# Performance work log

Hardware: AMD Instinct MI355X
Metric: run time of the kernel (lower is better)

The kernel has to match this reference:

```python
import jax, jax.numpy as jnp
import numpy as np
from jax import lax

H = 64          # num_heads
P = 64          # head_dim
N = 128         # ssm_state_size
G = 8           # n_groups
K = 4           # conv_kernel
D_MODEL = 4096  # hidden_size
I = H * P                      # intermediate_size = 4096
GN = G * N                     # groups_time_state_size = 1024
CONV_DIM = I + 2 * GN          # 6144
PROJ = I + CONV_DIM + H        # 10304
EPS = 1e-5
GROUP_SIZE = I // G            # 512


def setup_inputs() -> dict:
    key = jax.random.key(0)
    ks = jax.random.split(key, 6)
    B, L = 2, 2048
    s = 0.02
    return {
        "hidden_states": jax.random.normal(ks[0], (B, L, D_MODEL), jnp.float32),
        "in_proj_w": jax.random.normal(ks[1], (PROJ, D_MODEL), jnp.float32) * s,
        "conv_weight": jax.random.normal(ks[2], (CONV_DIM, K), jnp.float32) * s,
        "conv_bias": jnp.zeros((CONV_DIM,), jnp.float32),
        "dt_bias": jnp.ones((H,), jnp.float32),
        "A_log": jnp.log(jnp.arange(1, H + 1, dtype=jnp.float32)),
        "D": jnp.ones((H,), jnp.float32),
        "norm_weight": jnp.ones((I,), jnp.float32),
        "out_proj_w": jax.random.normal(ks[3], (D_MODEL, I), jnp.float32) * s,
    }


def reference(hidden_states, in_proj_w, conv_weight, conv_bias, dt_bias, A_log, D, norm_weight, out_proj_w):
    B, L, _ = hidden_states.shape

    # in_proj, then split into gate / conv-stream / dt
    proj = jnp.einsum("bld,pd->blp", hidden_states, in_proj_w)
    gate = proj[..., :I]
    hbc = proj[..., I:I + CONV_DIM]          # (B, L, conv_dim), pre-conv
    dt = proj[..., -H:]                       # (B, L, H)

    # depthwise causal conv1d + SiLU
    pad = jnp.pad(hbc, ((0, 0), (K - 1, 0), (0, 0)))
    conv = conv_bias
    for k in range(K):  # K=4, tiny fixed loop
        conv = conv + pad[:, k:k + L, :] * conv_weight[:, k]
    xBC = jax.nn.silu(conv)

    x = xBC[..., :I].reshape(B, L, H, P)                        # (B,L,H,P)
    Bm = xBC[..., I:I + GN].reshape(B, L, G, N)
    Cm = xBC[..., I + GN:].reshape(B, L, G, N)
    hpg = H // G
    B_h = jnp.repeat(Bm, hpg, axis=2)                            # (B,L,H,N)
    C_h = jnp.repeat(Cm, hpg, axis=2)                            # (B,L,H,N)

    # dt processing: softplus(dt + dt_bias), limits (0, inf)
    dt_p = jax.nn.softplus(dt + dt_bias)                         # (B,L,H)
    A = -jnp.exp(A_log)                                          # (H,)
    dA = jnp.exp(dt_p * A)                                       # (B,L,H)
    dtx = dt_p[..., None] * x                                    # (B,L,H,P)

    # selective scan over sequence (O(L)), state: (B,H,P,N)
    def step(state, inp):
        dA_t, dtx_t, B_t, C_t = inp
        state = state * dA_t[..., None, None] + dtx_t[..., None] * B_t[:, :, None, :]
        y_t = jnp.einsum("bhpn,bhn->bhp", state, C_t)
        return state, y_t

    xs = (jnp.moveaxis(dA, 1, 0), jnp.moveaxis(dtx, 1, 0),
          jnp.moveaxis(B_h, 1, 0), jnp.moveaxis(C_h, 1, 0))
    state0 = jnp.zeros((B, H, P, N), jnp.float32)
    final_state, ys = lax.scan(step, state0, xs)
    y = jnp.moveaxis(ys, 0, 1) + x * D[None, None, :, None]      # (B,L,H,P)
    y = y.reshape(B, L, I)

    # gated grouped RMSNorm: 8 independent RMSNorms over 512 elems each
    yg = y.reshape(B, L, G, GROUP_SIZE)
    var = jnp.mean(yg * yg, axis=-1, keepdims=True)
    yn = (yg * lax.rsqrt(var + EPS)).reshape(B, L, I) * norm_weight
    yn = yn * jax.nn.silu(gate)

    out = jnp.einsum("bli,di->bld", yn, out_proj_w)

    conv_state_new = jnp.moveaxis(hbc[:, L - (K - 1):, :], 1, 2)  # (B, conv_dim, K-1)
    return out, conv_state_new, final_state
```

## Files before the change

### kernel.cpp

```cpp
#include <hip/hip_runtime.h>
#include <cstdint>
#include <cstddef>

typedef __bf16 bf16;
typedef float f32x4 __attribute__((ext_vector_type(4)));
typedef bf16 bf16x8 __attribute__((ext_vector_type(8)));
typedef bf16 bf16x4 __attribute__((ext_vector_type(4)));

#define DM    4096
#define LL    2048
#define BB    2
#define BT    4096
#define II    4096
#define GN_   1024
#define CONVD 6144
#define PROJD 10304
#define NPAD  10496
#define HH    64
#define PP    64
#define NN    128
#define CT    64
#define NC    32

#define OUT_OFS_CONV  16777216
#define OUT_OFS_STATE 16814080

#define WS_HSB    0UL
#define WS_WINB   33554432UL
#define WS_DSB    0UL
#define WS_PROJ   119537664UL
#define WS_XBC    291504128UL
#define WS_DTDA   392167424UL
#define WS_Y      394264576UL
#define WS_WOUTB  0UL
#define WS_YNB    33554432UL

__device__ __forceinline__ void gl2lds16(const void* g, void* l) {
  __builtin_amdgcn_global_load_lds(
      (__attribute__((address_space(1))) unsigned int*)(uintptr_t)g,
      (__attribute__((address_space(3))) unsigned int*)(uintptr_t)l, 16, 0, 0);
}

__global__ __launch_bounds__(256) void cast2_kernel(const float* __restrict__ s1,
                                                    bf16* __restrict__ d1,
                                                    const float* __restrict__ s2,
                                                    bf16* __restrict__ d2,
                                                    long nsrc2, long ndst2) {
  if (blockIdx.x < 16384) {
    long i = ((long)blockIdx.x * 256 + threadIdx.x) * 4;
    float4 v = *(const float4*)(s1 + i);
    bf16x4 o;
    o[0] = (bf16)v.x; o[1] = (bf16)v.y; o[2] = (bf16)v.z; o[3] = (bf16)v.w;
    *(bf16x4*)(d1 + i) = o;
  } else {
    long i = ((long)(blockIdx.x - 16384) * 256 + threadIdx.x) * 4;
    if (i >= ndst2) return;
    bf16x4 o;
    if (i < nsrc2) {
      float4 v = *(const float4*)(s2 + i);
      o[0] = (bf16)v.x; o[1] = (bf16)v.y; o[2] = (bf16)v.z; o[3] = (bf16)v.w;
    } else {
      o[0] = (bf16)0.f; o[1] = (bf16)0.f; o[2] = (bf16)0.f; o[3] = (bf16)0.f;
    }
    *(bf16x4*)(d2 + i) = o;
  }
}

__global__ __launch_bounds__(256) void cast_kernel(const float* __restrict__ src,
                                                   bf16* __restrict__ dst,
                                                   long nsrc, long ndst) {
  long i = ((long)blockIdx.x * 256 + threadIdx.x) * 4;
  if (i >= ndst) return;
  bf16x4 o;
  if (i < nsrc) {
    float4 v = *(const float4*)(src + i);
    o[0] = (bf16)v.x; o[1] = (bf16)v.y; o[2] = (bf16)v.z; o[3] = (bf16)v.w;
  } else {
    o[0] = (bf16)0.f; o[1] = (bf16)0.f; o[2] = (bf16)0.f; o[3] = (bf16)0.f;
  }
  *(bf16x4*)(dst + i) = o;
}

#define BARF() do { asm volatile("" ::: "memory");                    \
                    __builtin_amdgcn_s_barrier();                     \
                    asm volatile("" ::: "memory"); } while (0)
#define WAITLGKM0() do { asm volatile("s_waitcnt lgkmcnt(0)" ::: "memory"); \
                         __builtin_amdgcn_sched_barrier(0); } while (0)
#define HINTLGKM8() asm volatile("s_waitcnt lgkmcnt(8)" ::: "memory")
#define WAITVM(n) asm volatile("s_waitcnt vmcnt(" #n ")" ::: "memory")
#define PRIO1 __builtin_amdgcn_s_setprio(1)
#define PRIO0 __builtin_amdgcn_s_setprio(0)

__device__ __forceinline__ void stage_A_half(const bf16* __restrict__ A, int K,
                                             int arow, int kt, bf16* lds,
                                             int h, int tid) {
#pragma unroll
  for (int j = 0; j < 2; ++j) {
    const int r  = h * 64 + j * 128 + (tid >> 3);
    const int cb = (tid & 7) * 16;
    const int cs = cb ^ ((r & 7) << 4);
    gl2lds16(A + (size_t)(arow + r) * K + kt * 64 + (cs >> 1),
             lds + r * 64 + (cb >> 1));
  }
}
__device__ __forceinline__ void stage_B_half(const bf16* __restrict__ B, int K,
                                             int brow, int kt, bf16* lds,
                                             int h, int tid) {
#pragma unroll
  for (int j = 0; j < 2; ++j) {
    const int quarter = j * 2 + (tid >> 8);
    const int kq = tid & 255;
    const int r  = quarter * 64 + h * 32 + (kq >> 3);
    const int cb = (kq & 7) * 16;
    const int cs = cb ^ ((r & 7) << 4);
    gl2lds16(B + (size_t)(brow + r) * K + kt * 64 + (cs >> 1),
             lds + r * 64 + (cb >> 1));
  }
}

#define LDA4(p, mh) do {                                                     \
  _Pragma("unroll") for (int mt = 0; mt < 4; ++mt)                           \
  _Pragma("unroll") for (int kk = 0; kk < 2; ++kk) {                         \
    const int rr = wm * 128 + (mh) * 64 + mt * 16 + l16;                     \
    const int cc = (kk * 64 + quad * 16) ^ ((rr & 7) << 4);                  \
    a_[mt][kk] = *(const bf16x8*)((const char*)(&sA[p][rr][0]) + cc);        \
  } } while (0)

#define LDB2(p, np, barr) do {                                               \
  _Pragma("unroll") for (int nt = 0; nt < 2; ++nt)                           \
  _Pragma("unroll") for (int kk = 0; kk < 2; ++kk) {                         \
    const int rr = wn * 64 + (np) * 32 + nt * 16 + l16;                      \
    const int cc = (kk * 64 + quad * 16) ^ ((rr & 7) << 4);                  \
    barr[nt][kk] = *(const bf16x8*)((const char*)(&sB[p][rr][0]) + cc);      \
  } } while (0)

#define MFMAQ(mh, barr, nb0) do {                                            \
  _Pragma("unroll") for (int kk = 0; kk < 2; ++kk)                           \
  _Pragma("unroll") for (int mt = 0; mt < 4; ++mt)                           \
  _Pragma("unroll") for (int nt = 0; nt < 2; ++nt)                           \
    acc[(mh) * 4 + mt][(nb0) + nt] = __builtin_amdgcn_mfma_f32_16x16x32_bf16(\
        a_[mt][kk], barr[nt][kk], acc[(mh) * 4 + mt][(nb0) + nt], 0, 0, 0);  \
  } while (0)

__global__ __launch_bounds__(512, 2) void gemm256(const bf16* __restrict__ A,
                                                  const bf16* __restrict__ B,
                                                  float* __restrict__ C,
                                                  int M, int N, int K, int NB) {
  __shared__ __align__(16) bf16 sA[2][256][64];
  __shared__ __align__(16) bf16 sB[2][256][64];

  const int tid  = threadIdx.x;
  const int wave = tid >> 6, lane = tid & 63;
  const int l16  = lane & 15, quad = lane >> 4;
  const int wm   = wave >> 2, wn = wave & 3;

  const int nwg = gridDim.x;
  const int q = nwg >> 3, r8 = nwg & 7;
  const int xcd = blockIdx.x & 7, idx = blockIdx.x >> 3;
  const int wgid = (xcd < r8 ? xcd * (q + 1) : r8 * (q + 1) + (xcd - r8) * q) + idx;
  const int mb = wgid / NB, nb = wgid - mb * NB;
  const int arow = mb * 256, brow = nb * 256;

  f32x4 acc[8][4];
#pragma unroll
  for (int i = 0; i < 8; ++i)
#pragma unroll
    for (int j = 0; j < 4; ++j) acc[i][j] = (f32x4)0.f;

  const int NT = K >> 6;

  stage_A_half(A, K, arow, 0, &sA[0][0][0], 0, tid);
  stage_B_half(B, K, brow, 0, &sB[0][0][0], 0, tid);
  stage_A_half(A, K, arow, 0, &sA[0][0][0], 1, tid);
  stage_B_half(B, K, brow, 0, &sB[0][0][0], 1, tid);
  stage_A_half(A, K, arow, 1, &sA[1][0][0], 0, tid);
  stage_B_half(B, K, brow, 1, &sB[1][0][0], 0, tid);
  stage_A_half(A, K, arow, 1, &sA[1][0][0], 1, tid);
  WAITVM(6);
  BARF();

  bf16x8 a_[4][2], b0_[2][2], b1_[2][2];

  for (int i = 0; i < NT / 2; ++i) {
    const int t1o = 2 * i + 1;
    const int t2  = (2 * i + 2 < NT) ? 2 * i + 2 : NT - 1;
    const int t3  = (2 * i + 3 < NT) ? 2 * i + 3 : NT - 1;

    LDA4(0, 0); LDB2(0, 0, b0_);
    stage_B_half(B, K, brow, t1o, &sB[1][0][0], 1, tid);
    HINTLGKM8();
    BARF(); WAITLGKM0();
    PRIO1; MFMAQ(0, b0_, 0); PRIO0;
    BARF();
    LDB2(0, 1, b1_);
    stage_A_half(A, K, arow, t2, &sA[0][0][0], 0, tid);
    BARF(); WAITLGKM0();
    PRIO1; MFMAQ(0, b1_, 2); PRIO0;
    BARF();
    LDA4(0, 1);
    stage_B_half(B, K, brow, t2, &sB[0][0][0], 0, tid);
    BARF(); WAITLGKM0();
    PRIO1; MFMAQ(1, b1_, 2); PRIO0;
    BARF();
    stage_A_half(A, K, arow, t2, &sA[0][0][0], 1, tid);
    WAITVM(6);
    BARF();
    PRIO1; MFMAQ(1, b0_, 0); PRIO0;
    BARF();
    LDA4(1, 0); LDB2(1, 0, b0_);
    stage_B_half(B, K, brow, t2, &sB[0][0][0], 1, tid);
    HINTLGKM8();
    BARF(); WAITLGKM0();
    PRIO1; MFMAQ(0, b0_, 0); PRIO0;
    BARF();
    LDB2(1, 1, b1_);
    stage_A_half(A, K, arow, t3, &sA[1][0][0], 0, tid);
    BARF(); WAITLGKM0();
    PRIO1; MFMAQ(0, b1_, 2); PRIO0;
    BARF();
    LDA4(1, 1);
    stage_B_half(B, K, brow, t3, &sB[1][0][0], 0, tid);
    BARF(); WAITLGKM0();
    PRIO1; MFMAQ(1, b1_, 2); PRIO0;
    BARF();
    stage_A_half(A, K, arow, t3, &sA[1][0][0], 1, tid);
    WAITVM(6);
    BARF();
    PRIO1; MFMAQ(1, b0_, 0); PRIO0;
    BARF();
  }
  asm volatile("s_waitcnt vmcnt(0)" ::: "memory");
  __builtin_amdgcn_s_barrier();

#pragma unroll
  for (int mt = 0; mt < 8; ++mt) {
    const int row0 = arow + wm * 128 + mt * 16 + quad * 4;
#pragma unroll
    for (int nt = 0; nt < 4; ++nt) {
      const int col = brow + wn * 64 + nt * 16 + l16;
#pragma unroll
      for (int r = 0; r < 4; ++r)
        C[(size_t)(row0 + r) * N + col] = acc[mt][nt][r];
    }
  }
}

#define CTILE 64
__global__ __launch_bounds__(256) void conv_kernel(const float* __restrict__ proj,
                                                   const float* __restrict__ cw,
                                                   const float* __restrict__ cb,
                                                   bf16* __restrict__ xbc) {
  const int c   = blockIdx.x * 256 + threadIdx.x;
  const int bt0 = blockIdx.y * CTILE;
  const int t0  = bt0 & (LL - 1);
  const float4 w = *(const float4*)(cw + c * 4);
  const float bias = cb[c];
  const float* p = proj + (size_t)bt0 * NPAD + II + c;
  float h0, h1, h2;
  if (t0 == 0) {
    h0 = 0.f; h1 = 0.f; h2 = 0.f;
  } else {
    h0 = p[-3 * (ptrdiff_t)NPAD];
    h1 = p[-2 * (ptrdiff_t)NPAD];
    h2 = p[-(ptrdiff_t)NPAD];
  }
  bf16* q = xbc + (size_t)bt0 * CONVD + c;
#pragma unroll 8
  for (int t = 0; t < CTILE; ++t) {
    const float cur = p[(ptrdiff_t)t * NPAD];
    const float acc = bias + h0 * w.x + h1 * w.y + h2 * w.z + cur * w.w;
    q[(size_t)t * CONVD] = (bf16)(acc / (1.f + __expf(-acc)));
    h0 = h1; h1 = h2; h2 = cur;
  }
}

__global__ __launch_bounds__(256) void dtcs_kernel(const float* __restrict__ proj,
                                                   const float* __restrict__ dt_bias,
                                                   const float* __restrict__ A_log,
                                                   float* __restrict__ dtda,
                                                   float* __restrict__ outp) {
  const int bid = blockIdx.x;
  if (bid < 1024) {
    const int idx = bid * 256 + threadIdx.x;
    const int bt = idx >> 6, h = idx & 63;
    const float z = proj[(size_t)bt * NPAD + (II + CONVD) + h] + dt_bias[h];
    const float sp = (z > 20.f) ? z : log1pf(__expf(z));
    const float a = -__expf(A_log[h]);
    float2 o; o.x = sp; o.y = __expf(sp * a);
    *(float2*)(dtda + (size_t)idx * 2) = o;
  } else {
    const int idx = (bid - 1024) * 256 + threadIdx.x;
    if (idx >= BB * CONVD * 3) return;
    const int b = idx / (CONVD * 3);
    const int r = idx - b * CONVD * 3;
    const int c = r / 3, j = r - c * 3;
    outp[idx] = proj[((size_t)b * LL + (LL - 3 + j)) * NPAD + II + c];
  }
}

#define SCAN_DECODE()                                                  \
  const int lin = blockIdx.x;                                          \
  const int hh  = (lin >> 3) & 7;                                      \
  const int id  = (lin & 7) | ((lin >> 6) << 3);                       \
  const int g   = id >> 6, c = (id >> 1) & 31, b = id & 1;             \
  const int h   = g * 8 + hh;

__global__ __launch_bounds__(256) void chunkA_kernel(const bf16* __restrict__ xbc,
                                                     const float* __restrict__ dtda,
                                                     const float* __restrict__ A_log,
                                                     float* __restrict__ ybuf,
                                                     bf16* __restrict__ dsb) {
  SCAN_DECODE();
  const int tid = threadIdx.x;
  const int wave = tid >> 6, lane = tid & 63;
  const int l16 = lane & 15, quad = lane >> 4;

  __shared__ __align__(16) bf16 CsBt[8192];
  __shared__ __align__(16) bf16 Bs[64][128];
  __shared__ __align__(16) bf16 Xt[64][64];
  __shared__ __align__(16) bf16 Ws[64][64];
  __shared__ float cums[64], dtps[64], wls[64];

  bf16 (*Cs)[128] = (bf16(*)[128])CsBt;
  bf16 (*Bt)[64]  = (bf16(*)[64])CsBt;

  const size_t rowbase = ((size_t)b * LL + (size_t)c * CT) * CONVD;

  {
    const int r0 = wave * 16;
    const bf16* gC = xbc + rowbase + (II + GN_) + g * 128;
    const bf16* gB = xbc + rowbase + II + g * 128;
#pragma unroll
    for (int j = 0; j < 4; ++j) {
      const int r  = r0 + j * 4 + (lane >> 4);
      const int ch = (lane & 15) ^ (r & 15);
      gl2lds16(gC + (size_t)r * CONVD + ch * 8, &Cs[r0 + j * 4][0]);
      gl2lds16(gB + (size_t)r * CONVD + ch * 8, &Bs[r0 + j * 4][0]);
    }
  }
  {
    const int j = tid >> 2, p0 = (tid & 3) * 16;
    const bf16* gpX = xbc + rowbase + (size_t)j * CONVD + h * 64 + p0;
#pragma unroll
    for (int k = 0; k < 2; ++k) {
      bf16x8 v = *(const bf16x8*)(gpX + k * 8);
#pragma unroll
      for (int e = 0; e < 8; ++e) {
        const int pp = p0 + k * 8 + e;
        Xt[pp][(((j >> 3) ^ (pp & 7)) * 8) + (j & 7)] = v[e];
      }
    }
  }
  if (wave == 0) {
    const float Ah = -__expf(A_log[h]);
    float2 dd = *(const float2*)(dtda + ((size_t)((b * LL + c * CT + lane)) * 64 + h) * 2);
    float s = dd.x * Ah;
#pragma unroll
    for (int d = 1; d < 64; d <<= 1) {
      float v = __shfl_up(s, d);
      if (lane >= d) s += v;
    }
    const float tot = __shfl(s, 63);
    cums[lane] = s;
    dtps[lane] = dd.x;
    wls[lane]  = __expf(tot - s) * dd.x;
  }
  __syncthreads();

  const int mrow = wave * 16 + l16;
  {
    f32x4 accg[4];
#pragma unroll
    for (int nt = 0; nt < 4; ++nt) accg[nt] = (f32x4)0.f;
#pragma unroll
    for (int k0 = 0; k0 < 128; k0 += 32) {
      bf16x8 af = *(const bf16x8*)&Cs[mrow][(((k0 >> 3) + quad) ^ (mrow & 15)) * 8];
#pragma unroll
      for (int nt = 0; nt < 4; ++nt) {
        const int nrow = nt * 16 + l16;
        bf16x8 bfr = *(const bf16x8*)&Bs[nrow][(((k0 >> 3) + quad) ^ (nrow & 15)) * 8];
        accg[nt] = __builtin_amdgcn_mfma_f32_16x16x32_bf16(af, bfr, accg[nt], 0, 0, 0);
      }
    }
#pragma unroll
    for (int nt = 0; nt < 4; ++nt) {
      const int j = nt * 16 + l16;
#pragma unroll
      for (int r = 0; r < 4; ++r) {
        const int i = wave * 16 + quad * 4 + r;
        float v = 0.f;
        if (j <= i) v = accg[nt][r] * __expf(cums[i] - cums[j]) * dtps[j];
        Ws[i][(((j >> 3) ^ (i & 7)) * 8) + (j & 7)] = (bf16)v;
      }
    }
  }
  __syncthreads();

  {
    const int n = tid >> 1, j0 = (tid & 1) * 32;
#pragma unroll
    for (int k = 0; k < 4; ++k) {
      bf16x8 v;
#pragma unroll
      for (int e = 0; e < 8; ++e) {
        const int j = j0 + k * 8 + e;
        v[e] = Bs[j][(((n >> 3) ^ (j & 15)) * 8) + (n & 7)];
      }
      *(bf16x8*)(&Bt[n][((((j0 + k * 8) >> 3) ^ (n & 7)) * 8)]) = v;
    }
  }
  __syncthreads();

  f32x4 accy[4];
#pragma unroll
  for (int pt = 0; pt < 4; ++pt) accy[pt] = (f32x4)0.f;
#pragma unroll
  for (int k0 = 0; k0 < 64; k0 += 32) {
    bf16x8 af = *(const bf16x8*)&Ws[mrow][(((k0 >> 3) + quad) ^ (mrow & 7)) * 8];
#pragma unroll
    for (int pt = 0; pt < 4; ++pt) {
      const int prow = pt * 16 + l16;
      bf16x8 bfr = *(const bf16x8*)&Xt[prow][(((k0 >> 3) + quad) ^ (prow & 7)) * 8];
      accy[pt] = __builtin_amdgcn_mfma_f32_16x16x32_bf16(af, bfr, accy[pt], 0, 0, 0);
    }
  }

  f32x4 accs[8];
#pragma unroll
  for (int nt = 0; nt < 8; ++nt) accs[nt] = (f32x4)0.f;
#pragma unroll
  for (int k0 = 0; k0 < 64; k0 += 32) {
    bf16x8 axr = *(const bf16x8*)&Xt[mrow][(((k0 >> 3) + quad) ^ (mrow & 7)) * 8];
    bf16x8 ax;
#pragma unroll
    for (int e = 0; e < 8; ++e)
      ax[e] = (bf16)((float)axr[e] * wls[k0 + quad * 8 + e]);
#pragma unroll
    for (int nt = 0; nt < 8; ++nt) {
      const int nrow = nt * 16 + l16;
      bf16x8 bfr = *(const bf16x8*)&Bt[nrow][(((k0 >> 3) + quad) ^ (nrow & 7)) * 8];
      accs[nt] = __builtin_amdgcn_mfma_f32_16x16x32_bf16(ax, bfr, accs[nt], 0, 0, 0);
    }
  }

#pragma unroll
  for (int pt = 0; pt < 4; ++pt) {
#pragma unroll
    for (int r = 0; r < 4; ++r) {
      const int i = wave * 16 + quad * 4 + r;
      ybuf[((size_t)(b * LL + c * CT + i)) * II + h * 64 + pt * 16 + l16] = accy[pt][r];
    }
  }
  const size_t dbase = (((size_t)(b * HH + h)) * NC + c) * (CT * NN);
#pragma unroll
  for (int nt = 0; nt < 8; ++nt) {
#pragma unroll
    for (int r = 0; r < 4; ++r) {
      const int p = wave * 16 + quad * 4 + r;
      dsb[dbase + (size_t)p * NN + nt * 16 + l16] = (bf16)accs[nt][r];
    }
  }
}

__global__ __launch_bounds__(256) void chain_kernel(const float* __restrict__ dtda,
                                                    const float* __restrict__ A_log,
                                                    bf16* __restrict__ dsb,
                                                    float* __restrict__ fst) {
  const int blk = blockIdx.x;
  const int b = blk >> 8, h = (blk >> 2) & 63, qtr = blk & 3;
  const int tid = threadIdx.x, wave = tid >> 6, lane = tid & 63;
  __shared__ float DcL[NC];

  const float Ah = -__expf(A_log[h]);
#pragma unroll
  for (int cc = 0; cc < 8; ++cc) {
    const int c = wave * 8 + cc;
    float2 dd = *(const float2*)(dtda + ((size_t)(b * LL + c * CT + lane) * 64 + h) * 2);
    float a = dd.x * Ah;
#pragma unroll
    for (int m = 1; m <= 32; m <<= 1) a += __shfl_xor(a, m);
    if (lane == 0) DcL[c] = __expf(a);
  }

  const int local = qtr * 2048 + tid * 8;
  const size_t base = ((size_t)(b * HH + h)) * NC * (CT * NN) + local;
  float s[8];
#pragma unroll
  for (int e = 0; e < 8; ++e) s[e] = 0.f;

  bf16x8 d0 = *(const bf16x8*)(dsb + base);
  __syncthreads();

  for (int c = 0; c < NC; ++c) {
    bf16* p = dsb + base + (size_t)c * (CT * NN);
    bf16x8 dn;
    if (c + 1 < NC) dn = *(const bf16x8*)(p + (CT * NN));
    const float dc = DcL[c];
    bf16x8 o0;
#pragma unroll
    for (int e = 0; e < 8; ++e) o0[e] = (bf16)s[e];
    *(bf16x8*)(p) = o0;
#pragma unroll
    for (int e = 0; e < 8; ++e) s[e] = s[e] * dc + (float)d0[e];
    d0 = dn;
  }
  float* fp = fst + ((size_t)(b * HH + h)) * (PP * NN) + local;
#pragma unroll
  for (int k = 0; k < 2; ++k) {
    float4 v = { s[k * 4], s[k * 4 + 1], s[k * 4 + 2], s[k * 4 + 3] };
    *(float4*)(fp + k * 4) = v;
  }
}

__global__ __launch_bounds__(256) void chunkB_kernel(const bf16* __restrict__ xbc,
                                                     const float* __restrict__ dtda,
                                                     const float* __restrict__ A_log,
                                                     const float* __restrict__ Dv,
                                                     const bf16* __restrict__ spb,
                                                     float* __restrict__ ybuf) {
  SCAN_DECODE();
  const int tid = threadIdx.x;
  const int wave = tid >> 6, lane = tid & 63;
  const int l16 = lane & 15, quad = lane >> 4;

  __shared__ __align__(16) bf16 Cs[64][128];
  __shared__ __align__(16) bf16 Sp[64][128];
  __shared__ float es[64];

  const size_t rowbase = ((size_t)b * LL + (size_t)c * CT) * CONVD;
  {
    const int r0 = wave * 16;
    const bf16* gC = xbc + rowbase + (II + GN_) + g * 128;
    const bf16* gS = spb + (((size_t)(b * HH + h)) * NC + c) * (CT * NN);
#pragma unroll
    for (int j = 0; j < 4; ++j) {
      const int r  = r0 + j * 4 + (lane >> 4);
      const int ch = (lane & 15) ^ (r & 15);
      gl2lds16(gC + (size_t)r * CONVD + ch * 8, &Cs[r0 + j * 4][0]);
      gl2lds16(gS + (size_t)r * NN   + ch * 8, &Sp[r0 + j * 4][0]);
    }
  }
  if (wave == 0) {
    const float Ah = -__expf(A_log[h]);
    float2 dd = *(const float2*)(dtda + ((size_t)(b * LL + c * CT + lane) * 64 + h) * 2);
    float s = dd.x * Ah;
#pragma unroll
    for (int d = 1; d < 64; d <<= 1) {
      float v = __shfl_up(s, d);
      if (lane >= d) s += v;
    }
    es[lane] = __expf(s);
  }
  __syncthreads();

  const int mrow = wave * 16 + l16;
  f32x4 acc[4];
#pragma unroll
  for (int pt = 0; pt < 4; ++pt) acc[pt] = (f32x4)0.f;
#pragma unroll
  for (int k0 = 0; k0 < 128; k0 += 32) {
    bf16x8 af = *(const bf16x8*)&Cs[mrow][(((k0 >> 3) + quad) ^ (mrow & 15)) * 8];
#pragma unroll
    for (int pt = 0; pt < 4; ++pt) {
      const int prow = pt * 16 + l16;
      bf16x8 bfr = *(const bf16x8*)&Sp[prow][(((k0 >> 3) + quad) ^ (prow & 15)) * 8];
      acc[pt] = __builtin_amdgcn_mfma_f32_16x16x32_bf16(af, bfr, acc[pt], 0, 0, 0);
    }
  }

  const float Dh = Dv[h];
#pragma unroll
  for (int pt = 0; pt < 4; ++pt) {
#pragma unroll
    for (int r = 0; r < 4; ++r) {
      const int i = wave * 16 + quad * 4 + r;
      const int p = pt * 16 + l16;
      const size_t row = (size_t)(b * LL + c * CT + i);
      const size_t ya = row * II + h * 64 + p;
      const float xv = (float)xbc[row * CONVD + h * 64 + p];
      ybuf[ya] = acc[pt][r] * es[i] + ybuf[ya] + Dh * xv;
    }
  }
}

__global__ __launch_bounds__(256) void norm_kernel(const float* __restrict__ y,
                                                   const float* __restrict__ proj,
                                                   const float* __restrict__ nw,
                                                   bf16* __restrict__ yn) {
  const int bt = blockIdx.x, tid = threadIdx.x;
  const float* yr = y + (size_t)bt * II + tid * 16;
  float4 v[4];
  float ss = 0.f;
#pragma unroll
  for (int i = 0; i < 4; ++i) {
    v[i] = *(const float4*)(yr + i * 4);
    ss += v[i].x * v[i].x + v[i].y * v[i].y + v[i].z * v[i].z + v[i].w * v[i].w;
  }
#pragma unroll
  for (int m = 1; m <= 16; m <<= 1) ss += __shfl_xor(ss, m);
  const float rstd = rsqrtf(ss * (1.f / 512.f) + 1e-5f);

  const float* gr  = proj + (size_t)bt * NPAD + tid * 16;
  const float* nwr = nw + tid * 16;
  bf16x8 o0, o1;
#pragma unroll
  for (int i = 0; i < 4; ++i) {
    float4 gv = *(const float4*)(gr + i * 4);
    float4 nv = *(const float4*)(nwr + i * 4);
    const float* vv = (const float*)&v[i];
    const float* gg = (const float*)&gv;
    const float* nn = (const float*)&nv;
#pragma unroll
    for (int j = 0; j < 4; ++j) {
      const float gate = gg[j];
      const float val = vv[j] * rstd * nn[j] * (gate / (1.f + __expf(-gate)));
      if (i < 2) o0[i * 4 + j] = (bf16)val;
      else       o1[(i - 2) * 4 + j] = (bf16)val;
    }
  }
  bf16* dst = yn + (size_t)bt * II + tid * 16;
  *(bf16x8*)(dst)     = o0;
  *(bf16x8*)(dst + 8) = o1;
}

extern "C" void kernel_launch(void* const* d_in, const int* in_sizes, int n_in,
                              void* d_out, int out_size, void* d_ws, size_t ws_size,
                              hipStream_t stream) {
  const float* hs      = (const float*)d_in[0];
  const float* w_in    = (const float*)d_in[1];
  const float* cw      = (const float*)d_in[2];
  const float* cb      = (const float*)d_in[3];
  const float* dt_bias = (const float*)d_in[4];
  const float* A_log   = (const float*)d_in[5];
  const float* Dv      = (const float*)d_in[6];
  const float* nw      = (const float*)d_in[7];
  const float* w_out   = (const float*)d_in[8];

  char* ws = (char*)d_ws;
  bf16*  hsb   = (bf16*)(ws + WS_HSB);
  bf16*  winb  = (bf16*)(ws + WS_WINB);
  bf16*  dsb   = (bf16*)(ws + WS_DSB);
  float* proj  = (float*)(ws + WS_PROJ);
  bf16*  xbc   = (bf16*)(ws + WS_XBC);
  float* dtda  = (float*)(ws + WS_DTDA);
  float* ybuf  = (float*)(ws + WS_Y);
  bf16*  ynb   = (bf16*)(ws + WS_YNB);
  bf16*  woutb = (bf16*)(ws + WS_WOUTB);

  float* outp = (float*)d_out;

  cast2_kernel<<<58368, 256, 0, stream>>>(hs, hsb, w_in, winb,
                                          (long)PROJD * DM, (long)NPAD * DM);

  gemm256<<<(BT / 256) * (NPAD / 256), 512, 0, stream>>>(hsb, winb, proj, BT, NPAD, DM, NPAD / 256);

  conv_kernel<<<dim3(CONVD / 256, BT / CTILE), 256, 0, stream>>>(proj, cw, cb, xbc);
  dtcs_kernel<<<1168, 256, 0, stream>>>(proj, dt_bias, A_log, dtda, outp + OUT_OFS_CONV);

  chunkA_kernel<<<4096, 256, 0, stream>>>(xbc, dtda, A_log, ybuf, dsb);
  chain_kernel<<<BB * HH * 4, 256, 0, stream>>>(dtda, A_log, dsb, outp + OUT_OFS_STATE);
  chunkB_kernel<<<4096, 256, 0, stream>>>(xbc, dtda, A_log, Dv, dsb, ybuf);

  cast_kernel<<<16384, 256, 0, stream>>>(w_out, woutb, 16777216L, 16777216L);
  norm_kernel<<<BT, 256, 0, stream>>>(ybuf, proj, nw, ynb);

  gemm256<<<(BT / 256) * (DM / 256), 512, 0, stream>>>(ynb, woutb, outp, BT, DM, II, DM / 256);
}
```

Measured before the change: 962.2 us.

## Store projection in bf16 and fuse chunk output with grouped RMSNorm gating

```diff
diff --git a/kernel.cpp b/kernel.cpp
--- a/kernel.cpp
+++ b/kernel.cpp
@@ -28,12 +28,14 @@
 #define WS_HSB    0UL
 #define WS_WINB   33554432UL
 #define WS_DSB    0UL
+#define WS_YNB    67108864UL
 #define WS_PROJ   119537664UL
-#define WS_XBC    291504128UL
-#define WS_DTDA   392167424UL
-#define WS_Y      394264576UL
-#define WS_WOUTB  0UL
-#define WS_YNB    33554432UL
+#define WS_XBC    205520896UL
+#define WS_DTDA   255852544UL
+#define WS_Y      257949696UL
+#define WS_DTF    291504128UL
+#define WS_HBC3   292552704UL
+#define WS_WOUTB  292700160UL
 
 __device__ __forceinline__ void gl2lds16(const void* g, void* l) {
   __builtin_amdgcn_global_load_lds(
@@ -41,19 +43,22 @@
       (__attribute__((address_space(3))) unsigned int*)(uintptr_t)l, 16, 0, 0);
 }
 
-__global__ __launch_bounds__(256) void cast2_kernel(const float* __restrict__ s1,
+__global__ __launch_bounds__(256) void cast3_kernel(const float* __restrict__ s1,
                                                     bf16* __restrict__ d1,
                                                     const float* __restrict__ s2,
                                                     bf16* __restrict__ d2,
+                                                    const float* __restrict__ s3,
+                                                    bf16* __restrict__ d3,
                                                     long nsrc2, long ndst2) {
-  if (blockIdx.x < 16384) {
-    long i = ((long)blockIdx.x * 256 + threadIdx.x) * 4;
+  const int bid = blockIdx.x;
+  if (bid < 16384) {
+    long i = ((long)bid * 256 + threadIdx.x) * 4;
     float4 v = *(const float4*)(s1 + i);
     bf16x4 o;
     o[0] = (bf16)v.x; o[1] = (bf16)v.y; o[2] = (bf16)v.z; o[3] = (bf16)v.w;
     *(bf16x4*)(d1 + i) = o;
-  } else {
-    long i = ((long)(blockIdx.x - 16384) * 256 + threadIdx.x) * 4;
+  } else if (bid < 58368) {
+    long i = ((long)(bid - 16384) * 256 + threadIdx.x) * 4;
     if (i >= ndst2) return;
     bf16x4 o;
     if (i < nsrc2) {
@@ -63,22 +68,13 @@
       o[0] = (bf16)0.f; o[1] = (bf16)0.f; o[2] = (bf16)0.f; o[3] = (bf16)0.f;
     }
     *(bf16x4*)(d2 + i) = o;
-  }
-}
-
-__global__ __launch_bounds__(256) void cast_kernel(const float* __restrict__ src,
-                                                   bf16* __restrict__ dst,
-                                                   long nsrc, long ndst) {
-  long i = ((long)blockIdx.x * 256 + threadIdx.x) * 4;
-  if (i >= ndst) return;
-  bf16x4 o;
-  if (i < nsrc) {
-    float4 v = *(const float4*)(src + i);
+  } else {
+    long i = ((long)(bid - 58368) * 256 + threadIdx.x) * 4;
+    float4 v = *(const float4*)(s3 + i);
+    bf16x4 o;
     o[0] = (bf16)v.x; o[1] = (bf16)v.y; o[2] = (bf16)v.z; o[3] = (bf16)v.w;
-  } else {
-    o[0] = (bf16)0.f; o[1] = (bf16)0.f; o[2] = (bf16)0.f; o[3] = (bf16)0.f;
-  }
-  *(bf16x4*)(dst + i) = o;
+    *(bf16x4*)(d3 + i) = o;
+  }
 }
 
 #define BARF() do { asm volatile("" ::: "memory");                    \
@@ -142,10 +138,13 @@
         a_[mt][kk], barr[nt][kk], acc[(mh) * 4 + mt][(nb0) + nt], 0, 0, 0);  \
   } while (0)
 
+template <int MODE>
 __global__ __launch_bounds__(512, 2) void gemm256(const bf16* __restrict__ A,
                                                   const bf16* __restrict__ B,
-                                                  float* __restrict__ C,
-                                                  int M, int N, int K, int NB) {
+                                                  void* __restrict__ Cv,
+                                                  int M, int N, int K, int NB,
+                                                  float* __restrict__ dtf,
+                                                  float* __restrict__ hbc3) {
   __shared__ __align__(16) bf16 sA[2][256][64];
   __shared__ __align__(16) bf16 sB[2][256][64];
 
@@ -239,14 +238,26 @@
     for (int nt = 0; nt < 4; ++nt) {
       const int col = brow + wn * 64 + nt * 16 + l16;
 #pragma unroll
-      for (int r = 0; r < 4; ++r)
-        C[(size_t)(row0 + r) * N + col] = acc[mt][nt][r];
+      for (int r = 0; r < 4; ++r) {
+        const float v = acc[mt][nt][r];
+        const int row = row0 + r;
+        if constexpr (MODE == 0) {
+          ((float*)Cv)[(size_t)row * N + col] = v;
+        } else {
+          ((bf16*)Cv)[(size_t)row * N + col] = (bf16)v;
+          const int dc = col - (II + CONVD);
+          if (dc >= 0 && dc < 64) dtf[(size_t)row * 64 + dc] = v;
+          const int rr = row & (LL - 1);
+          if (rr >= LL - 3 && col >= II && col < II + CONVD)
+            hbc3[((size_t)(row >> 11) * 3 + (rr - (LL - 3))) * CONVD + (col - II)] = v;
+        }
+      }
     }
   }
 }
 
 #define CTILE 64
-__global__ __launch_bounds__(256) void conv_kernel(const float* __restrict__ proj,
+__global__ __launch_bounds__(256) void conv_kernel(const bf16* __restrict__ proj,
                                                    const float* __restrict__ cw,
                                                    const float* __restrict__ cb,
                                                    bf16* __restrict__ xbc) {
@@ -255,26 +266,27 @@
   const int t0  = bt0 & (LL - 1);
   const float4 w = *(const float4*)(cw + c * 4);
   const float bias = cb[c];
-  const float* p = proj + (size_t)bt0 * NPAD + II + c;
+  const bf16* p = proj + (size_t)bt0 * NPAD + II + c;
   float h0, h1, h2;
   if (t0 == 0) {
     h0 = 0.f; h1 = 0.f; h2 = 0.f;
   } else {
-    h0 = p[-3 * (ptrdiff_t)NPAD];
-    h1 = p[-2 * (ptrdiff_t)NPAD];
-    h2 = p[-(ptrdiff_t)NPAD];
+    h0 = (float)p[-3 * (ptrdiff_t)NPAD];
+    h1 = (float)p[-2 * (ptrdiff_t)NPAD];
+    h2 = (float)p[-(ptrdiff_t)NPAD];
   }
   bf16* q = xbc + (size_t)bt0 * CONVD + c;
 #pragma unroll 8
   for (int t = 0; t < CTILE; ++t) {
-    const float cur = p[(ptrdiff_t)t * NPAD];
+    const float cur = (float)p[(ptrdiff_t)t * NPAD];
     const float acc = bias + h0 * w.x + h1 * w.y + h2 * w.z + cur * w.w;
     q[(size_t)t * CONVD] = (bf16)(acc / (1.f + __expf(-acc)));
     h0 = h1; h1 = h2; h2 = cur;
   }
 }
 
-__global__ __launch_bounds__(256) void dtcs_kernel(const float* __restrict__ proj,
+__global__ __launch_bounds__(256) void dtcs_kernel(const float* __restrict__ dtf,
+                                                   const float* __restrict__ hbc3,
                                                    const float* __restrict__ dt_bias,
                                                    const float* __restrict__ A_log,
                                                    float* __restrict__ dtda,
@@ -282,8 +294,8 @@
   const int bid = blockIdx.x;
   if (bid < 1024) {
     const int idx = bid * 256 + threadIdx.x;
-    const int bt = idx >> 6, h = idx & 63;
-    const float z = proj[(size_t)bt * NPAD + (II + CONVD) + h] + dt_bias[h];
+    const int h = idx & 63;
+    const float z = dtf[idx] + dt_bias[h];
     const float sp = (z > 20.f) ? z : log1pf(__expf(z));
     const float a = -__expf(A_log[h]);
     float2 o; o.x = sp; o.y = __expf(sp * a);
@@ -294,7 +306,7 @@
     const int b = idx / (CONVD * 3);
     const int r = idx - b * CONVD * 3;
     const int c = r / 3, j = r - c * 3;
-    outp[idx] = proj[((size_t)b * LL + (LL - 3 + j)) * NPAD + II + c];
+    outp[idx] = hbc3[((size_t)b * 3 + j) * CONVD + c];
   }
 }
 
@@ -308,7 +320,7 @@
 __global__ __launch_bounds__(256) void chunkA_kernel(const bf16* __restrict__ xbc,
                                                      const float* __restrict__ dtda,
                                                      const float* __restrict__ A_log,
-                                                     float* __restrict__ ybuf,
+                                                     bf16* __restrict__ ybuf,
                                                      bf16* __restrict__ dsb) {
   SCAN_DECODE();
   const int tid = threadIdx.x;
@@ -448,7 +460,7 @@
 #pragma unroll
     for (int r = 0; r < 4; ++r) {
       const int i = wave * 16 + quad * 4 + r;
-      ybuf[((size_t)(b * LL + c * CT + i)) * II + h * 64 + pt * 16 + l16] = accy[pt][r];
+      ybuf[((size_t)(b * LL + c * CT + i)) * II + h * 64 + pt * 16 + l16] = (bf16)accy[pt][r];
     }
   }
   const size_t dbase = (((size_t)(b * HH + h)) * NC + c) * (CT * NN);
@@ -512,35 +524,52 @@
   }
 }
 
-__global__ __launch_bounds__(256) void chunkB_kernel(const bf16* __restrict__ xbc,
-                                                     const float* __restrict__ dtda,
-                                                     const float* __restrict__ A_log,
-                                                     const float* __restrict__ Dv,
-                                                     const bf16* __restrict__ spb,
-                                                     float* __restrict__ ybuf) {
-  SCAN_DECODE();
+__global__ __launch_bounds__(512) void chunkBN_kernel(const bf16* __restrict__ xbc,
+                                                      const float* __restrict__ dtda,
+                                                      const float* __restrict__ A_log,
+                                                      const float* __restrict__ Dv,
+                                                      const bf16* __restrict__ spb,
+                                                      const bf16* __restrict__ ybi,
+                                                      const bf16* __restrict__ proj,
+                                                      const float* __restrict__ nw,
+                                                      bf16* __restrict__ ynb) {
+  const int lin = blockIdx.x;
+  const int g = lin >> 6, c = (lin >> 1) & 31, b = lin & 1;
   const int tid = threadIdx.x;
-  const int wave = tid >> 6, lane = tid & 63;
+  const int w = tid >> 6, lane = tid & 63;
   const int l16 = lane & 15, quad = lane >> 4;
-
-  __shared__ __align__(16) bf16 Cs[64][128];
-  __shared__ __align__(16) bf16 Sp[64][128];
+  const int h = g * 8 + w;
+
+  __shared__ __align__(16) char LB[147456];
+  __shared__ float sums[8][64];
   __shared__ float es[64];
+  __shared__ float rstd[64];
+
+  bf16 (*Cs)[128] = (bf16(*)[128])LB;
+  bf16 (*Sp)[128] = (bf16(*)[128])(LB + 16384 + (size_t)w * 16384);
 
   const size_t rowbase = ((size_t)b * LL + (size_t)c * CT) * CONVD;
   {
-    const int r0 = wave * 16;
     const bf16* gC = xbc + rowbase + (II + GN_) + g * 128;
+#pragma unroll
+    for (int j = 0; j < 2; ++j) {
+      const int r  = w * 8 + j * 4 + (lane >> 4);
+      const int ch = (lane & 15) ^ (r & 15);
+      gl2lds16(gC + (size_t)r * CONVD + ch * 8, LB + (w * 8 + j * 4) * 256);
+    }
     const bf16* gS = spb + (((size_t)(b * HH + h)) * NC + c) * (CT * NN);
 #pragma unroll
-    for (int j = 0; j < 4; ++j) {
-      const int r  = r0 + j * 4 + (lane >> 4);
+    for (int j = 0; j < 16; ++j) {
+      const int r  = j * 4 + (lane >> 4);
       const int ch = (lane & 15) ^ (r & 15);
-      gl2lds16(gC + (size_t)r * CONVD + ch * 8, &Cs[r0 + j * 4][0]);
-      gl2lds16(gS + (size_t)r * NN   + ch * 8, &Sp[r0 + j * 4][0]);
-    }
-  }
-  if (wave == 0) {
+      gl2lds16(gS + (size_t)r * NN + ch * 8, LB + 16384 + w * 16384 + j * 1024);
+    }
+  }
+  if (w == 0) {
+    const float Ah = -__expf(A_log[h]);
+  }
+  __shared__ float esw[8][64];
+  {
     const float Ah = -__expf(A_log[h]);
     float2 dd = *(const float2*)(dtda + ((size_t)(b * LL + c * CT + lane) * 64 + h) * 2);
     float s = dd.x * Ah;
@@ -549,78 +578,108 @@
       float v = __shfl_up(s, d);
       if (lane >= d) s += v;
     }
-    es[lane] = __expf(s);
+    esw[w][lane] = __expf(s);
   }
   __syncthreads();
 
-  const int mrow = wave * 16 + l16;
-  f32x4 acc[4];
-#pragma unroll
-  for (int pt = 0; pt < 4; ++pt) acc[pt] = (f32x4)0.f;
+  f32x4 acc[4][4];
+#pragma unroll
+  for (int it = 0; it < 4; ++it)
+#pragma unroll
+    for (int pt = 0; pt < 4; ++pt) acc[it][pt] = (f32x4)0.f;
+
 #pragma unroll
   for (int k0 = 0; k0 < 128; k0 += 32) {
-    bf16x8 af = *(const bf16x8*)&Cs[mrow][(((k0 >> 3) + quad) ^ (mrow & 15)) * 8];
-#pragma unroll
-    for (int pt = 0; pt < 4; ++pt) {
-      const int prow = pt * 16 + l16;
-      bf16x8 bfr = *(const bf16x8*)&Sp[prow][(((k0 >> 3) + quad) ^ (prow & 15)) * 8];
-      acc[pt] = __builtin_amdgcn_mfma_f32_16x16x32_bf16(af, bfr, acc[pt], 0, 0, 0);
-    }
+    bf16x8 af[4], bfr[4];
+#pragma unroll
+    for (int it = 0; it < 4; ++it) {
+      const int rr = it * 16 + l16;
+      af[it]  = *(const bf16x8*)&Cs[rr][(((k0 >> 3) + quad) ^ (rr & 15)) * 8];
+      bfr[it] = *(const bf16x8*)&Sp[rr][(((k0 >> 3) + quad) ^ (rr & 15)) * 8];
+    }
+#pragma unroll
+    for (int it = 0; it < 4; ++it)
+#pragma unroll
+      for (int pt = 0; pt < 4; ++pt)
+        acc[it][pt] = __builtin_amdgcn_mfma_f32_16x16x32_bf16(af[it], bfr[pt], acc[it][pt], 0, 0, 0);
   }
 
   const float Dh = Dv[h];
-#pragma unroll
-  for (int pt = 0; pt < 4; ++pt) {
+  const size_t grow0 = (size_t)b * LL + (size_t)c * CT;
+#pragma unroll
+  for (int it = 0; it < 4; ++it)
+#pragma unroll
+    for (int pt = 0; pt < 4; ++pt)
+#pragma unroll
+      for (int r = 0; r < 4; ++r) {
+        const int row = it * 16 + quad * 4 + r;
+        const int colh = pt * 16 + l16;
+        const size_t gr = grow0 + row;
+        acc[it][pt][r] = acc[it][pt][r] * esw[w][row]
+                       + (float)ybi[gr * II + h * 64 + colh]
+                       + Dh * (float)xbc[gr * CONVD + h * 64 + colh];
+      }
+
+  float ssv[4][4];
+#pragma unroll
+  for (int it = 0; it < 4; ++it)
 #pragma unroll
     for (int r = 0; r < 4; ++r) {
-      const int i = wave * 16 + quad * 4 + r;
-      const int p = pt * 16 + l16;
-      const size_t row = (size_t)(b * LL + c * CT + i);
-      const size_t ya = row * II + h * 64 + p;
-      const float xv = (float)xbc[row * CONVD + h * 64 + p];
-      ybuf[ya] = acc[pt][r] * es[i] + ybuf[ya] + Dh * xv;
-    }
-  }
-}
-
-__global__ __launch_bounds__(256) void norm_kernel(const float* __restrict__ y,
-                                                   const float* __restrict__ proj,
-                                                   const float* __restrict__ nw,
-                                                   bf16* __restrict__ yn) {
-  const int bt = blockIdx.x, tid = threadIdx.x;
-  const float* yr = y + (size_t)bt * II + tid * 16;
-  float4 v[4];
-  float ss = 0.f;
-#pragma unroll
-  for (int i = 0; i < 4; ++i) {
-    v[i] = *(const float4*)(yr + i * 4);
-    ss += v[i].x * v[i].x + v[i].y * v[i].y + v[i].z * v[i].z + v[i].w * v[i].w;
-  }
-#pragma unroll
-  for (int m = 1; m <= 16; m <<= 1) ss += __shfl_xor(ss, m);
-  const float rstd = rsqrtf(ss * (1.f / 512.f) + 1e-5f);
-
-  const float* gr  = proj + (size_t)bt * NPAD + tid * 16;
-  const float* nwr = nw + tid * 16;
-  bf16x8 o0, o1;
-#pragma unroll
-  for (int i = 0; i < 4; ++i) {
-    float4 gv = *(const float4*)(gr + i * 4);
-    float4 nv = *(const float4*)(nwr + i * 4);
-    const float* vv = (const float*)&v[i];
-    const float* gg = (const float*)&gv;
-    const float* nn = (const float*)&nv;
-#pragma unroll
-    for (int j = 0; j < 4; ++j) {
-      const float gate = gg[j];
-      const float val = vv[j] * rstd * nn[j] * (gate / (1.f + __expf(-gate)));
-      if (i < 2) o0[i * 4 + j] = (bf16)val;
-      else       o1[(i - 2) * 4 + j] = (bf16)val;
-    }
-  }
-  bf16* dst = yn + (size_t)bt * II + tid * 16;
-  *(bf16x8*)(dst)     = o0;
-  *(bf16x8*)(dst + 8) = o1;
+      float s = 0.f;
+#pragma unroll
+      for (int pt = 0; pt < 4; ++pt) s += acc[it][pt][r] * acc[it][pt][r];
+#pragma unroll
+      for (int m = 1; m <= 8; m <<= 1) s += __shfl_xor(s, m);
+      ssv[it][r] = s;
+    }
+  if (l16 == 0) {
+#pragma unroll
+    for (int it = 0; it < 4; ++it)
+#pragma unroll
+      for (int r = 0; r < 4; ++r)
+        sums[w][it * 16 + quad * 4 + r] = ssv[it][r];
+  }
+  __syncthreads();
+
+  if (tid < 64) {
+    float tot = 0.f;
+#pragma unroll
+    for (int ww = 0; ww < 8; ++ww) tot += sums[ww][tid];
+    rstd[tid] = rsqrtf(tot * (1.f / 512.f) + 1e-5f);
+  }
+  float* yls = (float*)LB;
+#pragma unroll
+  for (int it = 0; it < 4; ++it)
+#pragma unroll
+    for (int pt = 0; pt < 4; ++pt)
+#pragma unroll
+      for (int r = 0; r < 4; ++r)
+        yls[(it * 16 + quad * 4 + r) * 516 + w * 64 + pt * 16 + l16] = acc[it][pt][r];
+  __syncthreads();
+
+  {
+    const int row = tid >> 3, ch = tid & 7;
+    const size_t gr = grow0 + row;
+    const float rs = rstd[row];
+#pragma unroll
+    for (int k = 0; k < 4; ++k) {
+      const int col = ch * 16 + k * 128;
+      const float* yl = yls + (size_t)row * 516 + col;
+      bf16x8 gv0 = *(const bf16x8*)(proj + gr * NPAD + g * 512 + col);
+      bf16x8 gv1 = *(const bf16x8*)(proj + gr * NPAD + g * 512 + col + 8);
+      bf16x8 o0, o1;
+#pragma unroll
+      for (int e = 0; e < 8; ++e) {
+        const float gf0 = (float)gv0[e];
+        const float gf1 = (float)gv1[e];
+        const float v0 = yl[e]     * rs * nw[g * 512 + col + e]     * (gf0 / (1.f + __expf(-gf0)));
+        const float v1 = yl[e + 8] * rs * nw[g * 512 + col + e + 8] * (gf1 / (1.f + __expf(-gf1)));
+        o0[e] = (bf16)v0; o1[e] = (bf16)v1;
+      }
+      *(bf16x8*)(ynb + gr * II + g * 512 + col)     = o0;
+      *(bf16x8*)(ynb + gr * II + g * 512 + col + 8) = o1;
+    }
+  }
 }
 
 extern "C" void kernel_launch(void* const* d_in, const int* in_sizes, int n_in,
@@ -640,29 +699,30 @@
   bf16*  hsb   = (bf16*)(ws + WS_HSB);
   bf16*  winb  = (bf16*)(ws + WS_WINB);
   bf16*  dsb   = (bf16*)(ws + WS_DSB);
-  float* proj  = (float*)(ws + WS_PROJ);
+  bf16*  ynb   = (bf16*)(ws + WS_YNB);
+  bf16*  proj  = (bf16*)(ws + WS_PROJ);
   bf16*  xbc   = (bf16*)(ws + WS_XBC);
   float* dtda  = (float*)(ws + WS_DTDA);
-  float* ybuf  = (float*)(ws + WS_Y);
-  bf16*  ynb   = (bf16*)(ws + WS_YNB);
+  bf16*  ybuf  = (bf16*)(ws + WS_Y);
+  float* dtf   = (float*)(ws + WS_DTF);
+  float* hbc3  = (float*)(ws + WS_HBC3);
   bf16*  woutb = (bf16*)(ws + WS_WOUTB);
 
   float* outp = (float*)d_out;
 
-  cast2_kernel<<<58368, 256, 0, stream>>>(hs, hsb, w_in, winb,
+  cast3_kernel<<<74752, 256, 0, stream>>>(hs, hsb, w_in, winb, w_out, woutb,
                                           (long)PROJD * DM, (long)NPAD * DM);
 
-  gemm256<<<(BT / 256) * (NPAD / 256), 512, 0, stream>>>(hsb, winb, proj, BT, NPAD, DM, NPAD / 256);
+  gemm256<1><<<(BT / 256) * (NPAD / 256), 512, 0, stream>>>(
+      hsb, winb, proj, BT, NPAD, DM, NPAD / 256, dtf, hbc3);
 
   conv_kernel<<<dim3(CONVD / 256, BT / CTILE), 256, 0, stream>>>(proj, cw, cb, xbc);
-  dtcs_kernel<<<1168, 256, 0, stream>>>(proj, dt_bias, A_log, dtda, outp + OUT_OFS_CONV);
+  dtcs_kernel<<<1168, 256, 0, stream>>>(dtf, hbc3, dt_bias, A_log, dtda, outp + OUT_OFS_CONV);
 
   chunkA_kernel<<<4096, 256, 0, stream>>>(xbc, dtda, A_log, ybuf, dsb);
   chain_kernel<<<BB * HH * 4, 256, 0, stream>>>(dtda, A_log, dsb, outp + OUT_OFS_STATE);
-  chunkB_kernel<<<4096, 256, 0, stream>>>(xbc, dtda, A_log, Dv, dsb, ybuf);
-
-  cast_kernel<<<16384, 256, 0, stream>>>(w_out, woutb, 16777216L, 16777216L);
-  norm_kernel<<<BT, 256, 0, stream>>>(ybuf, proj, nw, ynb);
-
-  gemm256<<<(BT / 256) * (DM / 256), 512, 0, stream>>>(ynb, woutb, outp, BT, DM, II, DM / 256);
-}
+  chunkBN_kernel<<<512, 512, 0, stream>>>(xbc, dtda, A_log, Dv, dsb, ybuf, proj, nw, ynb);
+
+  gemm256<0><<<(BT / 256) * (DM / 256), 512, 0, stream>>>(
+      ynb, woutb, outp, BT, DM, II, DM / 256, nullptr, nullptr);
+}
```

New measurement: 906.4 us. 5.8% less time.
